# Performance work log

Measured on AMD Instinct MI355X. Metric: run time of the kernel, lower is better.

Reference implementation:

```python
import jax, jax.numpy as jnp
import numpy as np

B = 16384

def _linear_params(key, out_dim, in_dim):
    k1, k2 = jax.random.split(key)
    s = 1.0 / np.sqrt(in_dim)
    W = jax.random.uniform(k1, (out_dim, in_dim), jnp.float32, -s, s)
    b = jax.random.uniform(k2, (out_dim,), jnp.float32, -s, s)
    return W, b

def setup_inputs() -> dict:
    key = jax.random.key(0)
    ks = jax.random.split(key, 6)
    x = jax.random.normal(ks[0], (B, 784), jnp.float32)
    conv_w = jax.random.normal(ks[1], (3, 3), jnp.float32)
    W1, b1 = _linear_params(ks[2], 1024, 26 * 26)
    W2, b2 = _linear_params(ks[3], 512, 1024)
    W3, b3 = _linear_params(ks[4], 256, 512)
    W4, b4 = _linear_params(ks[5], 10, 256)
    return {"x": x, "conv_w": conv_w, "W1": W1, "b1": b1, "W2": W2, "b2": b2,
            "W3": W3, "b3": b3, "W4": W4, "b4": b4}

def reference(x, conv_w, W1, b1, W2, b2, W3, b3, W4, b4):
    b = x.shape[0]
    img = x.reshape(b, 1, 28, 28)                       # NCHW
    kern = conv_w.reshape(1, 1, 3, 3)                   # OIHW; cross-correlation
    y = jax.lax.conv_general_dilated(img, kern, (1, 1), 'VALID')  # [B,1,26,26]
    h = y.reshape(b, 26 * 26)
    h = jax.nn.relu(h @ W1.T + b1)
    h = jax.nn.relu(h @ W2.T + b2)
    h = jax.nn.relu(h @ W3.T + b3)
    return h @ W4.T + b4                                # [B,10] logits
```

## Files before the change

kernel.cpp:

```cpp
#include <hip/hip_runtime.h>
#include <hip/hip_bf16.h>
#include <stdint.h>

#define BDIM 256

typedef __attribute__((ext_vector_type(8))) short short8;
typedef __attribute__((ext_vector_type(4))) float f32x4;

#define AS1 __attribute__((address_space(1)))
#define AS3 __attribute__((address_space(3)))
#define GLL16(g, s) __builtin_amdgcn_global_load_lds((AS1 const void*)(g), (AS3 void*)(s), 16, 0, 0)

__device__ __forceinline__ unsigned short f2bf(float f) {
  union { float f; unsigned u; } v; v.f = f;
  unsigned r = v.u + 0x7fffu + ((v.u >> 16) & 1u);
  return (unsigned short)(r >> 16);
}
__device__ __forceinline__ float bf2f(unsigned short u) {
  union { unsigned u; float f; } v; v.u = ((unsigned)u) << 16;
  return v.f;
}

__global__ __launch_bounds__(BDIM) void cast_pad_w1(const float* __restrict__ w,
                                                    unsigned short* __restrict__ o) {
  int idx = blockIdx.x * BDIM + threadIdx.x;
  if (idx >= 1024 * 704) return;
  int n = idx / 704, k = idx - n * 704;
  float v = (k < 676) ? w[n * 676 + k] : 0.f;
  o[idx] = f2bf(v);
}

__global__ __launch_bounds__(BDIM) void cast_plain(const float* __restrict__ w,
                                                   unsigned short* __restrict__ o, int count) {
  int idx = blockIdx.x * BDIM + threadIdx.x;
  if (idx < count) o[idx] = f2bf(w[idx]);
}

__global__ __launch_bounds__(BDIM) void conv3x3(const float* __restrict__ x,
                                                const float* __restrict__ cw,
                                                unsigned short* __restrict__ h0) {
  __shared__ float xs[784];
  __shared__ float w[9];
  int m = blockIdx.x;
  const float* xr = x + (size_t)m * 784;
  if (threadIdx.x < 9) w[threadIdx.x] = cw[threadIdx.x];
  for (int i = threadIdx.x; i < 784; i += BDIM) xs[i] = xr[i];
  __syncthreads();
  unsigned short* hr = h0 + (size_t)m * 704;
  for (int p = threadIdx.x; p < 704; p += BDIM) {
    float v = 0.f;
    if (p < 676) {
      int r = p / 26, c = p - r * 26;
      const float* xp = &xs[r * 28 + c];
      v = xp[0]  * w[0] + xp[1]  * w[1] + xp[2]  * w[2]
        + xp[28] * w[3] + xp[29] * w[4] + xp[30] * w[5]
        + xp[56] * w[6] + xp[57] * w[7] + xp[58] * w[8];
    }
    hr[p] = f2bf(v);
  }
}

template <int BM, int BN, int WGM, bool RELU>
__global__ __launch_bounds__(512, 2) void gemm_bt2(const unsigned short* __restrict__ A,
                                                   const unsigned short* __restrict__ Wt,
                                                   const float* __restrict__ bias,
                                                   unsigned short* __restrict__ Cb,
                                                   int M, int N, int K) {
  constexpr int WGN = 8 / WGM;
  constexpr int FM = BM / WGM / 16;
  constexpr int FN = BN / WGN / 16;
  constexpr int RA = BM / 64;
  constexpr int RB = BN / 64;
  __shared__ unsigned short lds[(size_t)(BM + BN) * 128];
  unsigned short* const Asb = lds;
  unsigned short* const Bsb = lds + 2 * BM * 64;

  const int tid = threadIdx.x;
  const int lane = tid & 63;
  const int wid = tid >> 6;
  const int nbm = M / BM;
  const int brow = (blockIdx.x % nbm) * BM;
  const int bcol = (blockIdx.x / nbm) * BN;

  const int srow = tid >> 3;
  const int sslot = (tid & 7) ^ (srow & 7);
  const unsigned short* gA = A + (size_t)(brow + srow) * K + sslot * 8;
  const unsigned short* gB = Wt + (size_t)(bcol + srow) * K + sslot * 8;
  const int sdst = tid * 8;

#define STAGE(buf, kt)                                                            \
  do {                                                                            \
    _Pragma("unroll")                                                             \
    for (int r = 0; r < RA; ++r)                                                  \
      GLL16(gA + (size_t)r * 64 * K + (size_t)(kt) * 64,                          \
            Asb + (buf) * BM * 64 + r * 4096 + sdst);                             \
    _Pragma("unroll")                                                             \
    for (int r = 0; r < RB; ++r)                                                  \
      GLL16(gB + (size_t)r * 64 * K + (size_t)(kt) * 64,                          \
            Bsb + (buf) * BN * 64 + r * 4096 + sdst);                             \
  } while (0)

  f32x4 acc[FM][FN] = {};

  const int fr = lane & 15;
  const int h = lane >> 4;
  const int fx = fr & 7;
  const int abase = (wid / WGN) * (FM * 16);
  const int bbase = (wid % WGN) * (FN * 16);

  const int nk = K >> 6;
  STAGE(0, 0);
  __syncthreads();
  int cur = 0;
  for (int kt = 0; kt < nk; ++kt) {
    if (kt + 1 < nk) STAGE(cur ^ 1, kt + 1);
#pragma unroll
    for (int s = 0; s < 2; ++s) {
      const int slot = (((s << 2) + h) ^ fx) << 3;
      short8 af[FM], bf[FN];
#pragma unroll
      for (int m = 0; m < FM; ++m)
        af[m] = *(const short8*)&Asb[cur * BM * 64 + (abase + m * 16 + fr) * 64 + slot];
#pragma unroll
      for (int n = 0; n < FN; ++n)
        bf[n] = *(const short8*)&Bsb[cur * BN * 64 + (bbase + n * 16 + fr) * 64 + slot];
#pragma unroll
      for (int m = 0; m < FM; ++m)
#pragma unroll
        for (int n = 0; n < FN; ++n)
          acc[m][n] = __builtin_amdgcn_mfma_f32_16x16x32_bf16(af[m], bf[n], acc[m][n], 0, 0, 0);
    }
    __syncthreads();
    cur ^= 1;
  }
#undef STAGE

  unsigned short* const scr = lds;
  const int lrow0 = abase + (h << 2);
  const int lcol0 = bbase + fr;
#pragma unroll
  for (int n = 0; n < FN; ++n) {
    const int col = lcol0 + n * 16;
    const float bv = bias[bcol + col];
#pragma unroll
    for (int m = 0; m < FM; ++m) {
#pragma unroll
      for (int j = 0; j < 4; ++j) {
        const int row = lrow0 + m * 16 + j;
        float v = acc[m][n][j] + bv;
        if (RELU) v = v > 0.f ? v : 0.f;
        scr[(row * BN + col) ^ ((row & 12) << 2)] = f2bf(v);
      }
    }
  }
  __syncthreads();
  constexpr int CPR = BN / 8;
  constexpr int TOT = BM * CPR;
#pragma unroll 2
  for (int i = tid; i < TOT; i += 512) {
    const int row = i / CPR, c = i % CPR;
    const int cs = c ^ ((row & 12) >> 1);
    short8 vv = *(const short8*)&scr[row * BN + cs * 8];
    *(short8*)(Cb + (size_t)(brow + row) * N + bcol + c * 8) = vv;
  }
}

__global__ __launch_bounds__(BDIM) void fc10(const unsigned short* __restrict__ h3,
                                             const float* __restrict__ W4,
                                             const float* __restrict__ b4,
                                             float* __restrict__ out) {
  int lane = threadIdx.x & 63;
  int wid = threadIdx.x >> 6;
  int m = blockIdx.x * 4 + wid;
  const unsigned short* hr = h3 + (size_t)m * 256 + lane * 4;
  uint64_t hv = *(const uint64_t*)hr;
  float e0 = bf2f((unsigned short)hv), e1 = bf2f((unsigned short)(hv >> 16));
  float e2 = bf2f((unsigned short)(hv >> 32)), e3 = bf2f((unsigned short)(hv >> 48));
#pragma unroll
  for (int n = 0; n < 10; ++n) {
    const float4 wv = *(const float4*)(W4 + n * 256 + lane * 4);
    float s = e0 * wv.x + e1 * wv.y + e2 * wv.z + e3 * wv.w;
#pragma unroll
    for (int off = 32; off > 0; off >>= 1) s += __shfl_xor(s, off);
    if (lane == n) out[(size_t)m * 10 + n] = s + b4[n];
  }
}

extern "C" void kernel_launch(void* const* d_in, const int* in_sizes, int n_in,
                              void* d_out, int out_size, void* d_ws, size_t ws_size,
                              hipStream_t stream) {
  const float* x  = (const float*)d_in[0];
  const float* cw = (const float*)d_in[1];
  const float* W1 = (const float*)d_in[2];
  const float* b1 = (const float*)d_in[3];
  const float* W2 = (const float*)d_in[4];
  const float* b2 = (const float*)d_in[5];
  const float* W3 = (const float*)d_in[6];
  const float* b3 = (const float*)d_in[7];
  const float* W4 = (const float*)d_in[8];
  const float* b4 = (const float*)d_in[9];
  float* out = (float*)d_out;

  char* ws = (char*)d_ws;
  unsigned short* h0  = (unsigned short*)(ws);
  unsigned short* h1  = (unsigned short*)(ws + 23068672);
  unsigned short* W1b = (unsigned short*)(ws + 23068672 + 33554432);
  unsigned short* W2b = W1b + 1024 * 704;
  unsigned short* W3b = W2b + 512 * 1024;
  unsigned short* h2  = h0;
  unsigned short* h3  = h1;

  cast_pad_w1<<<2816, BDIM, 0, stream>>>(W1, W1b);
  cast_plain<<<2048, BDIM, 0, stream>>>(W2, W2b, 512 * 1024);
  cast_plain<<<512, BDIM, 0, stream>>>(W3, W3b, 256 * 512);
  conv3x3<<<16384, BDIM, 0, stream>>>(x, cw, h0);

  gemm_bt2<256, 256, 2, true><<<(16384 / 256) * (1024 / 256), 512, 0, stream>>>(
      h0, W1b, b1, h1, 16384, 1024, 704);
  gemm_bt2<256, 128, 4, true><<<(16384 / 256) * (512 / 128), 512, 0, stream>>>(
      h1, W2b, b2, h2, 16384, 512, 1024);
  gemm_bt2<128, 128, 4, true><<<(16384 / 128) * (256 / 128), 512, 0, stream>>>(
      h2, W3b, b3, h3, 16384, 256, 512);
  fc10<<<16384 / 4, BDIM, 0, stream>>>(h3, W4, b4, out);
}
```

Before: 110.1 us.

## Shrink GEMM tiles to 256-thread blocks with K=32 steps and XCD-aware block mapping

Measured after the change: 123.5 us. 12.2% more time.

```diff
diff --git a/kernel.cpp b/kernel.cpp
--- a/kernel.cpp
+++ b/kernel.cpp
@@ -61,75 +61,77 @@
 }
 
 template <int BM, int BN, int WGM, bool RELU>
-__global__ __launch_bounds__(512, 2) void gemm_bt2(const unsigned short* __restrict__ A,
-                                                   const unsigned short* __restrict__ Wt,
-                                                   const float* __restrict__ bias,
-                                                   unsigned short* __restrict__ Cb,
-                                                   int M, int N, int K) {
-  constexpr int WGN = 8 / WGM;
+__global__ __launch_bounds__(BDIM, 4) void gemm_bt5(const unsigned short* __restrict__ A,
+                                                    const unsigned short* __restrict__ Wt,
+                                                    const float* __restrict__ bias,
+                                                    unsigned short* __restrict__ Cb,
+                                                    int M, int N, int K) {
+  constexpr int WGN = 4 / WGM;
   constexpr int FM = BM / WGM / 16;
   constexpr int FN = BN / WGN / 16;
   constexpr int RA = BM / 64;
   constexpr int RB = BN / 64;
-  __shared__ unsigned short lds[(size_t)(BM + BN) * 128];
+  __shared__ unsigned short lds[2 * (BM + BN) * 32];
   unsigned short* const Asb = lds;
-  unsigned short* const Bsb = lds + 2 * BM * 64;
+  unsigned short* const Bsb = lds + 2 * BM * 32;
 
   const int tid = threadIdx.x;
   const int lane = tid & 63;
   const int wid = tid >> 6;
-  const int nbm = M / BM;
-  const int brow = (blockIdx.x % nbm) * BM;
-  const int bcol = (blockIdx.x / nbm) * BN;
-
-  const int srow = tid >> 3;
-  const int sslot = (tid & 7) ^ (srow & 7);
+
+  const int nbm = M / BM, nbc = N / BN;
+  const int grid = nbm * nbc;
+  const int cpx = grid >> 3;
+  const int nid = ((int)blockIdx.x & 7) * cpx + ((int)blockIdx.x >> 3);
+  const int brow = (nid / nbc) * BM;
+  const int bcol = (nid % nbc) * BN;
+
+  const int srow = tid >> 2;
+  const int sslot = (tid & 3) ^ (srow & 3);
   const unsigned short* gA = A + (size_t)(brow + srow) * K + sslot * 8;
   const unsigned short* gB = Wt + (size_t)(bcol + srow) * K + sslot * 8;
   const int sdst = tid * 8;
 
-#define STAGE(buf, kt)                                                            \
-  do {                                                                            \
-    _Pragma("unroll")                                                             \
-    for (int r = 0; r < RA; ++r)                                                  \
-      GLL16(gA + (size_t)r * 64 * K + (size_t)(kt) * 64,                          \
-            Asb + (buf) * BM * 64 + r * 4096 + sdst);                             \
-    _Pragma("unroll")                                                             \
-    for (int r = 0; r < RB; ++r)                                                  \
-      GLL16(gB + (size_t)r * 64 * K + (size_t)(kt) * 64,                          \
-            Bsb + (buf) * BN * 64 + r * 4096 + sdst);                             \
+#define STAGE(buf, kt)                                                        \
+  do {                                                                        \
+    _Pragma("unroll")                                                         \
+    for (int r = 0; r < RA; ++r)                                              \
+      GLL16(gA + (size_t)r * 64 * K + (size_t)(kt) * 32,                      \
+            Asb + (buf) * BM * 32 + r * 2048 + sdst);                         \
+    _Pragma("unroll")                                                         \
+    for (int r = 0; r < RB; ++r)                                              \
+      GLL16(gB + (size_t)r * 64 * K + (size_t)(kt) * 32,                      \
+            Bsb + (buf) * BN * 32 + r * 2048 + sdst);                         \
   } while (0)
 
   f32x4 acc[FM][FN] = {};
-
   const int fr = lane & 15;
   const int h = lane >> 4;
-  const int fx = fr & 7;
+  const int fx = fr & 3;
   const int abase = (wid / WGN) * (FM * 16);
   const int bbase = (wid % WGN) * (FN * 16);
-
-  const int nk = K >> 6;
+  const int slot = (h ^ fx) << 3;
+
+  const int nk = K >> 5;
   STAGE(0, 0);
   __syncthreads();
   int cur = 0;
   for (int kt = 0; kt < nk; ++kt) {
     if (kt + 1 < nk) STAGE(cur ^ 1, kt + 1);
-#pragma unroll
-    for (int s = 0; s < 2; ++s) {
-      const int slot = (((s << 2) + h) ^ fx) << 3;
-      short8 af[FM], bf[FN];
-#pragma unroll
-      for (int m = 0; m < FM; ++m)
-        af[m] = *(const short8*)&Asb[cur * BM * 64 + (abase + m * 16 + fr) * 64 + slot];
+    const unsigned short* As0 = Asb + cur * BM * 32;
+    const unsigned short* Bs0 = Bsb + cur * BN * 32;
+    short8 af[FM], bf[FN];
+#pragma unroll
+    for (int m = 0; m < FM; ++m)
+      af[m] = *(const short8*)&As0[(abase + m * 16 + fr) * 32 + slot];
+#pragma unroll
+    for (int n = 0; n < FN; ++n)
+      bf[n] = *(const short8*)&Bs0[(bbase + n * 16 + fr) * 32 + slot];
+#pragma unroll
+    for (int m = 0; m < FM; ++m)
 #pragma unroll
       for (int n = 0; n < FN; ++n)
-        bf[n] = *(const short8*)&Bsb[cur * BN * 64 + (bbase + n * 16 + fr) * 64 + slot];
-#pragma unroll
-      for (int m = 0; m < FM; ++m)
-#pragma unroll
-        for (int n = 0; n < FN; ++n)
-          acc[m][n] = __builtin_amdgcn_mfma_f32_16x16x32_bf16(af[m], bf[n], acc[m][n], 0, 0, 0);
-    }
+        acc[m][n] = __builtin_amdgcn_mfma_f32_16x16x32_bf16(af[m], bf[n], acc[m][n], 0, 0, 0);
     __syncthreads();
     cur ^= 1;
   }
@@ -157,7 +159,7 @@
   constexpr int CPR = BN / 8;
   constexpr int TOT = BM * CPR;
 #pragma unroll 2
-  for (int i = tid; i < TOT; i += 512) {
+  for (int i = tid; i < TOT; i += BDIM) {
     const int row = i / CPR, c = i % CPR;
     const int cs = c ^ ((row & 12) >> 1);
     short8 vv = *(const short8*)&scr[row * BN + cs * 8];
@@ -215,11 +217,11 @@
   cast_plain<<<512, BDIM, 0, stream>>>(W3, W3b, 256 * 512);
   conv3x3<<<16384, BDIM, 0, stream>>>(x, cw, h0);
 
-  gemm_bt2<256, 256, 2, true><<<(16384 / 256) * (1024 / 256), 512, 0, stream>>>(
+  gemm_bt5<128, 128, 2, true><<<(16384 / 128) * (1024 / 128), BDIM, 0, stream>>>(
       h0, W1b, b1, h1, 16384, 1024, 704);
-  gemm_bt2<256, 128, 4, true><<<(16384 / 256) * (512 / 128), 512, 0, stream>>>(
+  gemm_bt5<64, 128, 1, true><<<(16384 / 64) * (512 / 128), BDIM, 0, stream>>>(
       h1, W2b, b2, h2, 16384, 512, 1024);
-  gemm_bt2<128, 128, 4, true><<<(16384 / 128) * (256 / 128), 512, 0, stream>>>(
+  gemm_bt5<64, 64, 2, true><<<(16384 / 64) * (256 / 64), BDIM, 0, stream>>>(
       h2, W3b, b3, h3, 16384, 256, 512);
   fc10<<<16384 / 4, BDIM, 0, stream>>>(h3, W4, b4, out);
 }
```
